# Performance work log

Measured on AMD Instinct MI355X. Metric: run time of the kernel, lower is better.

The kernel has to match this reference:

```python
import jax, jax.numpy as jnp
import numpy as np

FEATURE_COUNT = 40960
HIDDEN = 256
BATCH = 131072
BAG = 32  # active features per perspective (fixed-size bag)


def setup_inputs() -> dict:
    key = jax.random.key(0)
    ks = jax.random.split(key, 9)
    inp = {
        "indices_us": jax.random.randint(ks[0], (BATCH, BAG), 0, FEATURE_COUNT, dtype=jnp.int32),
        "indices_them": jax.random.randint(ks[1], (BATCH, BAG), 0, FEATURE_COUNT, dtype=jnp.int32),
        "emb_weight": jax.random.normal(ks[2], (FEATURE_COUNT, HIDDEN), dtype=jnp.float32) * 0.05,
        "l1_w": jax.random.normal(ks[3], (32, 2 * HIDDEN), dtype=jnp.float32) * 0.05,
        "l1_b": jax.random.normal(ks[4], (32,), dtype=jnp.float32) * 0.05,
        "l2_w": jax.random.normal(ks[5], (32, 32), dtype=jnp.float32) * 0.05,
        "l2_b": jax.random.normal(ks[6], (32,), dtype=jnp.float32) * 0.05,
        "out_w": jax.random.normal(ks[7], (1, 32), dtype=jnp.float32) * 0.05,
        "out_b": jax.random.normal(ks[8], (1,), dtype=jnp.float32) * 0.05,
    }
    return inp


def _clipped_relu(x):
    return jnp.clip(x, 0.0, 1.0)


def reference(indices_us, indices_them, emb_weight, l1_w, l1_b, l2_w, l2_b, out_w, out_b):
    # EmbeddingBag(mode='sum') with uniform bags of size BAG:
    # gather [B, BAG, H] then sum over bag dim -> [B, H]
    acc_us = emb_weight[indices_us].sum(axis=1)
    acc_them = emb_weight[indices_them].sum(axis=1)
    x = jnp.concatenate([acc_us, acc_them], axis=1)  # [B, 2H]
    x = _clipped_relu(x)
    x = _clipped_relu(x @ l1_w.T + l1_b)
    x = _clipped_relu(x @ l2_w.T + l2_b)
    return x @ out_w.T + out_b  # [B, 1]
```

## Files before the change

### kernel.cpp

```cpp
#include <hip/hip_runtime.h>
#include <hip/hip_fp16.h>


constexpr int kBatch  = 131072;
constexpr int kHidden = 256;
constexpr int kBag    = 32;
constexpr int kFeat   = 40960;

constexpr int    kSlices     = 8;
constexpr int    kSliceDims  = 32;
constexpr size_t kSliceBytes = (size_t)kFeat * kSliceDims * 2;
constexpr size_t kEmbsBytes  = kSliceBytes * kSlices;
constexpr size_t kXBytes     = (size_t)kBatch * 2 * kHidden * 2;

typedef unsigned u32x4 __attribute__((ext_vector_type(4)));

__device__ __forceinline__ float clip1(float x) {
  return fminf(fmaxf(x, 0.0f), 1.0f);
}

typedef _Float16 h2_t __attribute__((ext_vector_type(2)));

__device__ __forceinline__ unsigned pkadd(unsigned a, unsigned b) {
  const h2_t r = __builtin_bit_cast(h2_t, a) + __builtin_bit_cast(h2_t, b);
  return __builtin_bit_cast(unsigned, r);
}

__device__ __forceinline__ unsigned pkclip(unsigned a) {
  unsigned r;
  const unsigned zero = 0u;
  const unsigned one  = 0x3C003C00u;
  asm("v_pk_max_f16 %0, %1, %2\n\t"
      "v_pk_min_f16 %0, %0, %3"
      : "=&v"(r)
      : "v"(a), "v"(zero), "v"(one));
  return r;
}

__device__ __forceinline__ float fdot2w(unsigned a, unsigned b, float c) {
  return __builtin_amdgcn_fdot2(__builtin_bit_cast(h2_t, a),
                                __builtin_bit_cast(h2_t, b), c, false);
}

template <int D, int HALF>
__device__ __forceinline__ void rs_stage(float (&p)[32], int lane) {
  const bool up = (lane & D) != 0;
#pragma unroll
  for (int i = 0; i < HALF; ++i) {
    const float send = up ? p[i] : p[i + HALF];
    const float recv = __shfl_xor(send, D, 64);
    p[i] = (up ? p[i + HALF] : p[i]) + recv;
  }
}

__device__ __forceinline__ float reduce32(float (&p)[32], int lane) {
  rs_stage<32, 16>(p, lane);
  rs_stage<16, 8>(p, lane);
  rs_stage<8, 4>(p, lane);
  rs_stage<4, 2>(p, lane);
  rs_stage<2, 1>(p, lane);
  return p[0] + __shfl_xor(p[0], 1, 64);
}

__global__ void cvt_sliced(const float* __restrict__ src,
                           uint4* __restrict__ dst) {
  const int total  = kFeat * 32;
  const int stride = gridDim.x * blockDim.x;
  for (int T = blockIdx.x * blockDim.x + threadIdx.x; T < total; T += stride) {
    const int r = T >> 5, s = (T >> 2) & 7, q = T & 3;
    const float4* p = (const float4*)(src + (size_t)r * 256 + s * 32 + q * 8);
    const float4 fa = p[0], fb = p[1];
    uint4 o;
    o.x = __builtin_bit_cast(unsigned, __floats2half2_rn(fa.x, fa.y));
    o.y = __builtin_bit_cast(unsigned, __floats2half2_rn(fa.z, fa.w));
    o.z = __builtin_bit_cast(unsigned, __floats2half2_rn(fb.x, fb.y));
    o.w = __builtin_bit_cast(unsigned, __floats2half2_rn(fb.z, fb.w));
    dst[(size_t)(s * kFeat + r) * 4 + q] = o;
  }
}

__global__ void cvt_emb(const float4* __restrict__ src, uint2* __restrict__ dst) {
  const int n4 = kFeat * kHidden / 4;
  const int stride = gridDim.x * blockDim.x;
  for (int i = blockIdx.x * blockDim.x + threadIdx.x; i < n4; i += stride) {
    const float4 v = src[i];
    union { __half2 h[2]; uint2 u; } P;
    P.h[0] = __floats2half2_rn(v.x, v.y);
    P.h[1] = __floats2half2_rn(v.z, v.w);
    dst[i] = P.u;
  }
}

constexpr int kGBlocks  = 2048;
constexpr int kGTpb     = 256;
constexpr int kGChunk   = kBatch / (kGBlocks / kSlices);
constexpr int kGPerWave = kGChunk / 4;
static_assert(kGChunk * (kGBlocks / kSlices) == kBatch);
static_assert(kGPerWave % 4 == 0);

__device__ __forceinline__ void bag_reduce(const u32x4 v0, const u32x4 v1,
                                           const u32x4 v2, const u32x4 v3,
                                           int lane, unsigned& U, unsigned& T) {
  unsigned aU[4] = {pkadd(v0.x, v1.x), pkadd(v0.y, v1.y),
                    pkadd(v0.z, v1.z), pkadd(v0.w, v1.w)};
  unsigned aT[4] = {pkadd(v2.x, v3.x), pkadd(v2.y, v3.y),
                    pkadd(v2.z, v3.z), pkadd(v2.w, v3.w)};
  {
    const bool up = (lane & 4) != 0;
#pragma unroll
    for (int i = 0; i < 2; ++i) {
      unsigned sU = up ? aU[i] : aU[i + 2];
      unsigned sT = up ? aT[i] : aT[i + 2];
      sU = (unsigned)__shfl_xor((int)sU, 4, 64);
      sT = (unsigned)__shfl_xor((int)sT, 4, 64);
      aU[i] = pkadd(up ? aU[i + 2] : aU[i], sU);
      aT[i] = pkadd(up ? aT[i + 2] : aT[i], sT);
    }
  }
  {
    const bool up = (lane & 8) != 0;
    unsigned sU = up ? aU[0] : aU[1];
    unsigned sT = up ? aT[0] : aT[1];
    sU = (unsigned)__shfl_xor((int)sU, 8, 64);
    sT = (unsigned)__shfl_xor((int)sT, 8, 64);
    aU[0] = pkadd(up ? aU[1] : aU[0], sU);
    aT[0] = pkadd(up ? aT[1] : aT[0], sT);
  }
  aU[0] = pkadd(aU[0], (unsigned)__shfl_xor((int)aU[0], 16, 64));
  aT[0] = pkadd(aT[0], (unsigned)__shfl_xor((int)aT[0], 16, 64));
  aU[0] = pkadd(aU[0], (unsigned)__shfl_xor((int)aU[0], 32, 64));
  aT[0] = pkadd(aT[0], (unsigned)__shfl_xor((int)aT[0], 32, 64));
  U = aU[0];
  T = aT[0];
}

__global__ __launch_bounds__(kGTpb, 4) void nnue_gather(
    const int* __restrict__ idx_us, const int* __restrict__ idx_th,
    const __half* __restrict__ embs, __half* __restrict__ x) {
  const int s     = blockIdx.x & 7;
  const int chunk = blockIdx.x >> 3;
  const int t    = threadIdx.x;
  const int lane = t & 63;
  const int g = lane >> 2, q = lane & 3;
  const u32x4* sbase =
      (const u32x4*)((const char*)embs + (size_t)s * kSliceBytes);
  unsigned* xw = (unsigned*)x;

  const int d = q * 8 + ((lane >> 2) & 1) * 4 + ((lane >> 3) & 1) * 2;
  const int wordoff = (lane < 16 ? 0 : 128) + s * 16 + (d >> 1);

  const int b0w = chunk * kGChunk + (t >> 6) * kGPerWave;
  for (int e = 0; e < kGPerWave; e += 4) {
    const int bA = b0w + e, bB = bA + 1, bC = bA + 2, bD = bA + 3;
    const size_t oA = (size_t)bA * kBag, oB = (size_t)bB * kBag;
    const size_t oC = (size_t)bC * kBag, oD = (size_t)bD * kBag;

    const int uA0 = idx_us[oA + g], uA1 = idx_us[oA + 16 + g];
    const int tA0 = idx_th[oA + g], tA1 = idx_th[oA + 16 + g];
    const int uB0 = idx_us[oB + g], uB1 = idx_us[oB + 16 + g];
    const int tB0 = idx_th[oB + g], tB1 = idx_th[oB + 16 + g];
    const int uC0 = idx_us[oC + g], uC1 = idx_us[oC + 16 + g];
    const int tC0 = idx_th[oC + g], tC1 = idx_th[oC + 16 + g];
    const int uD0 = idx_us[oD + g], uD1 = idx_us[oD + 16 + g];
    const int tD0 = idx_th[oD + g], tD1 = idx_th[oD + 16 + g];

    const u32x4 vA0 = sbase[uA0 * 4 + q], vA1 = sbase[uA1 * 4 + q];
    const u32x4 vA2 = sbase[tA0 * 4 + q], vA3 = sbase[tA1 * 4 + q];
    const u32x4 vB0 = sbase[uB0 * 4 + q], vB1 = sbase[uB1 * 4 + q];
    const u32x4 vB2 = sbase[tB0 * 4 + q], vB3 = sbase[tB1 * 4 + q];
    const u32x4 vC0 = sbase[uC0 * 4 + q], vC1 = sbase[uC1 * 4 + q];
    const u32x4 vC2 = sbase[tC0 * 4 + q], vC3 = sbase[tC1 * 4 + q];
    const u32x4 vD0 = sbase[uD0 * 4 + q], vD1 = sbase[uD1 * 4 + q];
    const u32x4 vD2 = sbase[tD0 * 4 + q], vD3 = sbase[tD1 * 4 + q];

    unsigned UA, TA, UB, TB, UC, TC, UD, TD;
    bag_reduce(vA0, vA1, vA2, vA3, lane, UA, TA);
    bag_reduce(vB0, vB1, vB2, vB3, lane, UB, TB);
    bag_reduce(vC0, vC1, vC2, vC3, lane, UC, TC);
    bag_reduce(vD0, vD1, vD2, vD3, lane, UD, TD);

    if (lane < 32) {
      __builtin_nontemporal_store(pkclip(lane < 16 ? UA : TA),
                                  xw + (size_t)bA * 256 + wordoff);
      __builtin_nontemporal_store(pkclip(lane < 16 ? UB : TB),
                                  xw + (size_t)bB * 256 + wordoff);
      __builtin_nontemporal_store(pkclip(lane < 16 ? UC : TC),
                                  xw + (size_t)bC * 256 + wordoff);
      __builtin_nontemporal_store(pkclip(lane < 16 ? UD : TD),
                                  xw + (size_t)bD * 256 + wordoff);
    }
  }
}

constexpr int kMBlocks = 1024;
constexpr int kMTpb    = 256;
constexpr int kMWpb    = kMTpb / 64;
constexpr int kMElems  = kBatch / (kMBlocks * kMWpb);
static_assert(kBatch % (kMBlocks * kMWpb) == 0);

__global__ __launch_bounds__(kMTpb, 4) void nnue_mlp(
    const __half* __restrict__ x, const float* __restrict__ w1,
    const float* __restrict__ b1, const float* __restrict__ w2,
    const float* __restrict__ b2, const float* __restrict__ wo,
    const float* __restrict__ bo, float* __restrict__ out) {
  __shared__ __align__(16) __half sW1h[32 * 512];
  __shared__ __align__(16) __half sY1h[kMWpb][2][32];

  const int t = threadIdx.x;
  {
    const float4* src = (const float4*)w1;
#pragma unroll
    for (int c = 0; c < 16; ++c) {
      const float4 v = src[t * 16 + c];
      __half2* d = (__half2*)&sW1h[t * 64 + 4 * c];
      d[0] = __floats2half2_rn(v.x, v.y);
      d[1] = __floats2half2_rn(v.z, v.w);
    }
  }
  __syncthreads();

  const int lane   = t & 63;
  const int wlocal = t >> 6;
  const int wid    = blockIdx.x * kMWpb + wlocal;
  const int myj    = lane >> 1;
  const int j2     = lane & 31;

  const float b1r  = b1[myj];
  const float b2r  = b2[j2];
  const float wor  = wo[j2];
  const float outb = bo[0];
  unsigned w2h[16];
#pragma unroll
  for (int k = 0; k < 16; ++k) {
    w2h[k] = __builtin_bit_cast(
        unsigned, __floats2half2_rn(w2[j2 * 32 + 2 * k], w2[j2 * 32 + 2 * k + 1]));
  }

  const u32x4* xq = (const u32x4*)x;
  for (int e = 0; e < kMElems; e += 2) {
    const int b0 = wid * kMElems + e;
    const int b1i = b0 + 1;
    const u32x4 xv0 = __builtin_nontemporal_load(xq + (size_t)b0 * 64 + lane);
    const u32x4 xv1 = __builtin_nontemporal_load(xq + (size_t)b1i * 64 + lane);

    float p0[32], p1[32];
#pragma unroll
    for (int j = 0; j < 32; ++j) {
      const uint4 wv = *(const uint4*)&sW1h[(j * 64 + lane) * 8];
      float s0 = fdot2w(wv.x, xv0.x, 0.0f);
      float s1 = fdot2w(wv.x, xv1.x, 0.0f);
      s0 = fdot2w(wv.y, xv0.y, s0);
      s1 = fdot2w(wv.y, xv1.y, s1);
      s0 = fdot2w(wv.z, xv0.z, s0);
      s1 = fdot2w(wv.z, xv1.z, s1);
      s0 = fdot2w(wv.w, xv0.w, s0);
      s1 = fdot2w(wv.w, xv1.w, s1);
      p0[j] = s0;
      p1[j] = s1;
    }
    const float y10 = clip1(reduce32(p0, lane) + b1r);
    const float y11 = clip1(reduce32(p1, lane) + b1r);

    if ((lane & 1) == 0) {
      sY1h[wlocal][0][myj] = __float2half(y10);
      sY1h[wlocal][1][myj] = __float2half(y11);
    }
    asm volatile("s_waitcnt lgkmcnt(0)" ::: "memory");

    const uint4* yv0 = (const uint4*)&sY1h[wlocal][0][0];
    const uint4* yv1 = (const uint4*)&sY1h[wlocal][1][0];
    float y20 = b2r, y21 = b2r;
#pragma unroll
    for (int k4 = 0; k4 < 4; ++k4) {
      const uint4 ya = yv0[k4];
      const uint4 yb = yv1[k4];
      y20 = fdot2w(w2h[4 * k4 + 0], ya.x, y20);
      y21 = fdot2w(w2h[4 * k4 + 0], yb.x, y21);
      y20 = fdot2w(w2h[4 * k4 + 1], ya.y, y20);
      y21 = fdot2w(w2h[4 * k4 + 1], yb.y, y21);
      y20 = fdot2w(w2h[4 * k4 + 2], ya.z, y20);
      y21 = fdot2w(w2h[4 * k4 + 2], yb.z, y21);
      y20 = fdot2w(w2h[4 * k4 + 3], ya.w, y20);
      y21 = fdot2w(w2h[4 * k4 + 3], yb.w, y21);
    }
    y20 = clip1(y20);
    y21 = clip1(y21);

    float a0 = y20 * wor;
    float a1 = y21 * wor;
#pragma unroll
    for (int d = 1; d < 32; d <<= 1) {
      a0 += __shfl_xor(a0, d, 64);
      a1 += __shfl_xor(a1, d, 64);
    }
    if (lane == 0) {
      out[b0]  = a0 + outb;
      out[b1i] = a1 + outb;
    }
  }
}

constexpr int kBlocksH = 1024;
constexpr int kTpb     = 256;
constexpr int kWpb     = kTpb / 64;
constexpr int kElemsH  = kBatch / (kBlocksH * kWpb);
constexpr int kPairs   = kElemsH / 2;

__device__ __forceinline__ void mlp_tail(
    const __half* __restrict__ sW1h, __half* __restrict__ sy1row,
    const unsigned (&x2)[4], const unsigned (&w2h)[16],
    float b1r, float b2r, float wor, float outb,
    int lane, int myj, float* __restrict__ out, int b) {
  float p[32];
#pragma unroll
  for (int j = 0; j < 32; ++j) {
    const uint4 wv = *(const uint4*)&sW1h[(j * 64 + lane) * 8];
    float s = fdot2w(wv.x, x2[0], 0.0f);
    s = fdot2w(wv.y, x2[1], s);
    s = fdot2w(wv.z, x2[2], s);
    s = fdot2w(wv.w, x2[3], s);
    p[j] = s;
  }
  const float y1 = clip1(reduce32(p, lane) + b1r);

  if ((lane & 1) == 0) sy1row[myj] = __float2half(y1);
  asm volatile("s_waitcnt lgkmcnt(0)" ::: "memory");

  const uint4* yv = (const uint4*)sy1row;
  float y2 = b2r;
#pragma unroll
  for (int k4 = 0; k4 < 4; ++k4) {
    const uint4 y = yv[k4];
    y2 = fdot2w(w2h[4 * k4 + 0], y.x, y2);
    y2 = fdot2w(w2h[4 * k4 + 1], y.y, y2);
    y2 = fdot2w(w2h[4 * k4 + 2], y.z, y2);
    y2 = fdot2w(w2h[4 * k4 + 3], y.w, y2);
  }
  y2 = clip1(y2);

  float acc = y2 * wor;
#pragma unroll
  for (int d = 1; d < 32; d <<= 1) acc += __shfl_xor(acc, d, 64);
  if (lane == 0) out[b] = acc + outb;
}

__global__ __launch_bounds__(kTpb, 4) void nnue_fwd_h(
    const int* __restrict__ idx_us, const int* __restrict__ idx_th,
    const __half* __restrict__ embh, const float* __restrict__ w1,
    const float* __restrict__ b1, const float* __restrict__ w2,
    const float* __restrict__ b2, const float* __restrict__ wo,
    const float* __restrict__ bo, float* __restrict__ out) {
  __shared__ __align__(16) __half sW1h[32 * 512];
  __shared__ __align__(16) __half sY1h[kWpb][32];

  const int t = threadIdx.x;
  {
    const float4* src = (const float4*)w1;
#pragma unroll
    for (int c = 0; c < 16; ++c) {
      const float4 v = src[t * 16 + c];
      __half2* d = (__half2*)&sW1h[t * 64 + 4 * c];
      d[0] = __floats2half2_rn(v.x, v.y);
      d[1] = __floats2half2_rn(v.z, v.w);
    }
  }
  __syncthreads();

  const int lane    = t & 63;
  const int wlocal  = t >> 6;
  const int wid     = blockIdx.x * kWpb + wlocal;
  const int myj     = lane >> 1;
  const int j2      = lane & 31;
  const int half31  = lane & 31;
  const bool hiHalf = lane >= 32;
  const uint4* embq = (const uint4*)embh;

  const float b1r  = b1[myj];
  const float b2r  = b2[j2];
  const float wor  = wo[j2];
  const float outb = bo[0];
  unsigned w2h[16];
#pragma unroll
  for (int k = 0; k < 16; ++k) {
    w2h[k] = __builtin_bit_cast(
        unsigned, __floats2half2_rn(w2[j2 * 32 + 2 * k], w2[j2 * 32 + 2 * k + 1]));
  }

  for (int e = 0; e < kPairs; ++e) {
    const int b0 = wid * kElemsH + 2 * e;
    const int b1i = b0 + 1;
    const int* ip0 = (lane < kBag) ? (idx_us + (size_t)b0 * kBag + lane)
                                   : (idx_th + (size_t)b0 * kBag + (lane - kBag));
    const int* ip1 = (lane < kBag) ? (idx_us + (size_t)b1i * kBag + lane)
                                    : (idx_th + (size_t)b1i * kBag + (lane - kBag));
    const int vidx0 = *ip0;
    const int vidx1 = *ip1;

    unsigned A0[8] = {0, 0, 0, 0, 0, 0, 0, 0};
    unsigned T0[8] = {0, 0, 0, 0, 0, 0, 0, 0};
    unsigned A1[8] = {0, 0, 0, 0, 0, 0, 0, 0};
    unsigned T1[8] = {0, 0, 0, 0, 0, 0, 0, 0};
#pragma unroll
    for (int s = 0; s < 16; ++s) {
      const int r0A = __builtin_amdgcn_readlane(vidx0, 2 * s);
      const int r0B = __builtin_amdgcn_readlane(vidx0, 2 * s + 1);
      const int r1A = __builtin_amdgcn_readlane(vidx1, 2 * s);
      const int r1B = __builtin_amdgcn_readlane(vidx1, 2 * s + 1);
      const uint4 v0 = embq[(size_t)(hiHalf ? r0B : r0A) * 32 + half31];
      const uint4 v1 = embq[(size_t)(hiHalf ? r1B : r1A) * 32 + half31];
      const int o = (s & 1) * 4;
      A0[o + 0] = pkadd(A0[o + 0], v0.x);
      A0[o + 1] = pkadd(A0[o + 1], v0.y);
      A0[o + 2] = pkadd(A0[o + 2], v0.z);
      A0[o + 3] = pkadd(A0[o + 3], v0.w);
      A1[o + 0] = pkadd(A1[o + 0], v1.x);
      A1[o + 1] = pkadd(A1[o + 1], v1.y);
      A1[o + 2] = pkadd(A1[o + 2], v1.z);
      A1[o + 3] = pkadd(A1[o + 3], v1.w);
    }
#pragma unroll
    for (int s = 0; s < 16; ++s) {
      const int r0A = __builtin_amdgcn_readlane(vidx0, 32 + 2 * s);
      const int r0B = __builtin_amdgcn_readlane(vidx0, 33 + 2 * s);
      const int r1A = __builtin_amdgcn_readlane(vidx1, 32 + 2 * s);
      const int r1B = __builtin_amdgcn_readlane(vidx1, 33 + 2 * s);
      const uint4 v0 = embq[(size_t)(hiHalf ? r0B : r0A) * 32 + half31];
      const uint4 v1 = embq[(size_t)(hiHalf ? r1B : r1A) * 32 + half31];
      const int o = (s & 1) * 4;
      T0[o + 0] = pkadd(T0[o + 0], v0.x);
      T0[o + 1] = pkadd(T0[o + 1], v0.y);
      T0[o + 2] = pkadd(T0[o + 2], v0.z);
      T0[o + 3] = pkadd(T0[o + 3], v0.w);
      T1[o + 0] = pkadd(T1[o + 0], v1.x);
      T1[o + 1] = pkadd(T1[o + 1], v1.y);
      T1[o + 2] = pkadd(T1[o + 2], v1.z);
      T1[o + 3] = pkadd(T1[o + 3], v1.w);
    }

    unsigned x20[4], x21[4];
#pragma unroll
    for (int q = 0; q < 4; ++q) {
      unsigned u0 = pkadd(A0[q], A0[q + 4]);
      unsigned t0 = pkadd(T0[q], T0[q + 4]);
      unsigned u1 = pkadd(A1[q], A1[q + 4]);
      unsigned t1 = pkadd(T1[q], T1[q + 4]);
      u0 = pkadd(u0, (unsigned)__shfl_xor((int)u0, 32, 64));
      t0 = pkadd(t0, (unsigned)__shfl_xor((int)t0, 32, 64));
      u1 = pkadd(u1, (unsigned)__shfl_xor((int)u1, 32, 64));
      t1 = pkadd(t1, (unsigned)__shfl_xor((int)t1, 32, 64));
      x20[q] = pkclip(hiHalf ? t0 : u0);
      x21[q] = pkclip(hiHalf ? t1 : u1);
    }

    mlp_tail(sW1h, &sY1h[wlocal][0], x20, w2h, b1r, b2r, wor, outb, lane, myj,
             out, b0);
    mlp_tail(sW1h, &sY1h[wlocal][0], x21, w2h, b1r, b2r, wor, outb, lane, myj,
             out, b1i);
  }
}

constexpr int kTpbF    = 256;
constexpr int kWpbF    = kTpbF / 64;
constexpr int kBlocksF = 512;
constexpr int kElemsF  = kBatch / (kBlocksF * kWpbF);

__global__ __launch_bounds__(kTpbF, 2) void nnue_fwd_f32(
    const int* __restrict__ idx_us, const int* __restrict__ idx_th,
    const float* __restrict__ emb, const float* __restrict__ w1,
    const float* __restrict__ b1, const float* __restrict__ w2,
    const float* __restrict__ b2, const float* __restrict__ wo,
    const float* __restrict__ bo, float* __restrict__ out) {
  __shared__ float sW1[32][512];
  __shared__ __align__(16) float sY1[kWpbF][32];

  const int t = threadIdx.x;
  {
    const float4* src = (const float4*)w1;
    float4* dst = (float4*)&sW1[0][0];
#pragma unroll
    for (int i = 0; i < 16; ++i) dst[i * kTpbF + t] = src[i * kTpbF + t];
  }
  __syncthreads();

  const int lane   = t & 63;
  const int wlocal = t >> 6;
  const int wid    = blockIdx.x * kWpbF + wlocal;
  const int myj    = lane >> 1;
  const int j2     = lane & 31;

  const float b1r  = b1[myj];
  const float b2r  = b2[j2];
  const float wor  = wo[j2];
  const float outb = bo[0];
  float w2r[32];
#pragma unroll
  for (int k = 0; k < 32; ++k) w2r[k] = w2[j2 * 32 + k];

  for (int e = 0; e < kElemsF; ++e) {
    const int b = wid * kElemsF + e;
    const int* ip = (lane < kBag) ? (idx_us + (size_t)b * kBag + lane)
                                  : (idx_th + (size_t)b * kBag + (lane - kBag));
    const int vidx = *ip;

    float4 au = make_float4(0.f, 0.f, 0.f, 0.f);
    float4 at = make_float4(0.f, 0.f, 0.f, 0.f);
#pragma unroll
    for (int i = 0; i < kBag; ++i) {
      const int iu = __builtin_amdgcn_readlane(vidx, i);
      const float4 v = ((const float4*)(emb + (size_t)iu * kHidden))[lane];
      au.x += v.x; au.y += v.y; au.z += v.z; au.w += v.w;
    }
#pragma unroll
    for (int i = 0; i < kBag; ++i) {
      const int it2 = __builtin_amdgcn_readlane(vidx, i + kBag);
      const float4 v = ((const float4*)(emb + (size_t)it2 * kHidden))[lane];
      at.x += v.x; at.y += v.y; at.z += v.z; at.w += v.w;
    }

    au.x = clip1(au.x); au.y = clip1(au.y); au.z = clip1(au.z); au.w = clip1(au.w);
    at.x = clip1(at.x); at.y = clip1(at.y); at.z = clip1(at.z); at.w = clip1(at.w);

    float p[32];
#pragma unroll
    for (int j = 0; j < 32; ++j) {
      const float4 a = *(const float4*)&sW1[j][4 * lane];
      const float4 c = *(const float4*)&sW1[j][kHidden + 4 * lane];
      p[j] = au.x * a.x + au.y * a.y + au.z * a.z + au.w * a.w +
             at.x * c.x + at.y * c.y + at.z * c.z + at.w * c.w;
    }
    const float y1 = clip1(reduce32(p, lane) + b1r);

    if ((lane & 1) == 0) sY1[wlocal][myj] = y1;
    asm volatile("s_waitcnt lgkmcnt(0)" ::: "memory");

    const float4* y4 = (const float4*)&sY1[wlocal][0];
    float y2 = b2r;
#pragma unroll
    for (int k4 = 0; k4 < 8; ++k4) {
      const float4 y = y4[k4];
      y2 += w2r[4 * k4 + 0] * y.x + w2r[4 * k4 + 1] * y.y +
            w2r[4 * k4 + 2] * y.z + w2r[4 * k4 + 3] * y.w;
    }
    y2 = clip1(y2);

    float acc = y2 * wor;
#pragma unroll
    for (int d = 1; d < 32; d <<= 1) acc += __shfl_xor(acc, d, 64);
    if (lane == 0) out[b] = acc + outb;
  }
}

extern "C" void kernel_launch(void* const* d_in, const int* in_sizes, int n_in,
                              void* d_out, int out_size, void* d_ws, size_t ws_size,
                              hipStream_t stream) {
  const int* idx_us  = (const int*)d_in[0];
  const int* idx_th  = (const int*)d_in[1];
  const float* emb   = (const float*)d_in[2];
  const float* w1    = (const float*)d_in[3];
  const float* b1    = (const float*)d_in[4];
  const float* w2    = (const float*)d_in[5];
  const float* b2    = (const float*)d_in[6];
  const float* wo    = (const float*)d_in[7];
  const float* bo    = (const float*)d_in[8];
  float* out         = (float*)d_out;

  if (ws_size >= kEmbsBytes + kXBytes) {
    __half* embs = (__half*)d_ws;
    __half* x    = (__half*)((char*)d_ws + kEmbsBytes);
    cvt_sliced<<<2560, 256, 0, stream>>>(emb, (uint4*)embs);
    nnue_gather<<<kGBlocks, kGTpb, 0, stream>>>(idx_us, idx_th, embs, x);
    nnue_mlp<<<kMBlocks, kMTpb, 0, stream>>>(x, w1, b1, w2, b2, wo, bo, out);
  } else if (ws_size >= kEmbsBytes) {
    __half* embh = (__half*)d_ws;
    cvt_emb<<<2048, 256, 0, stream>>>((const float4*)emb, (uint2*)embh);
    nnue_fwd_h<<<kBlocksH, kTpb, 0, stream>>>(idx_us, idx_th, embh, w1, b1, w2,
                                              b2, wo, bo, out);
  } else {
    nnue_fwd_f32<<<kBlocksF, kTpbF, 0, stream>>>(idx_us, idx_th, emb, w1, b1,
                                                 w2, b2, wo, bo, out);
  }
}
```

Baseline: 404.2 us.

## Software-pipeline gather loads across element pairs and double MLP grid blocks

Restructures the gather loop into a two-stage software pipeline: the loads for the next pair of batch elements are issued before the current pair is reduced and stored, so memory latency overlaps with the shuffle reductions. On the last iteration it prefetches element 0 again, a wasted load. It also doubles the MLP kernel's block count, halving the elements per wave and meaning the W1 staging into shared memory is repeated by twice as many blocks. Register pressure rises from holding two pairs of loaded vectors at once.

```diff
diff --git a/kernel.cpp b/kernel.cpp
--- a/kernel.cpp
+++ b/kernel.cpp
@@ -134,6 +134,41 @@
   T = aT[0];
 }
 
+__device__ __forceinline__ void g_load2(const int* __restrict__ idx_us,
+                                        const int* __restrict__ idx_th,
+                                        const u32x4* __restrict__ sbase,
+                                        int g, int q, int bA, u32x4 (&V)[8]) {
+  const int bB = bA + 1;
+  const size_t oA = (size_t)bA * kBag, oB = (size_t)bB * kBag;
+  const int uA0 = idx_us[oA + g], uA1 = idx_us[oA + 16 + g];
+  const int tA0 = idx_th[oA + g], tA1 = idx_th[oA + 16 + g];
+  const int uB0 = idx_us[oB + g], uB1 = idx_us[oB + 16 + g];
+  const int tB0 = idx_th[oB + g], tB1 = idx_th[oB + 16 + g];
+  V[0] = sbase[uA0 * 4 + q];
+  V[1] = sbase[uA1 * 4 + q];
+  V[2] = sbase[tA0 * 4 + q];
+  V[3] = sbase[tA1 * 4 + q];
+  V[4] = sbase[uB0 * 4 + q];
+  V[5] = sbase[uB1 * 4 + q];
+  V[6] = sbase[tB0 * 4 + q];
+  V[7] = sbase[tB1 * 4 + q];
+}
+
+__device__ __forceinline__ void g_finish2(const u32x4 (&V)[8], int lane,
+                                          int bA, unsigned* __restrict__ xw,
+                                          int wordoff) {
+  const int bB = bA + 1;
+  unsigned UA, TA, UB, TB;
+  bag_reduce(V[0], V[1], V[2], V[3], lane, UA, TA);
+  bag_reduce(V[4], V[5], V[6], V[7], lane, UB, TB);
+  if (lane < 32) {
+    __builtin_nontemporal_store(pkclip(lane < 16 ? UA : TA),
+                                xw + (size_t)bA * 256 + wordoff);
+    __builtin_nontemporal_store(pkclip(lane < 16 ? UB : TB),
+                                xw + (size_t)bB * 256 + wordoff);
+  }
+}
+
 __global__ __launch_bounds__(kGTpb, 4) void nnue_gather(
     const int* __restrict__ idx_us, const int* __restrict__ idx_th,
     const __half* __restrict__ embs, __half* __restrict__ x) {
@@ -150,49 +185,20 @@
   const int wordoff = (lane < 16 ? 0 : 128) + s * 16 + (d >> 1);
 
   const int b0w = chunk * kGChunk + (t >> 6) * kGPerWave;
+
+  u32x4 P[8], Q[8];
+  g_load2(idx_us, idx_th, sbase, g, q, b0w, P);
   for (int e = 0; e < kGPerWave; e += 4) {
-    const int bA = b0w + e, bB = bA + 1, bC = bA + 2, bD = bA + 3;
-    const size_t oA = (size_t)bA * kBag, oB = (size_t)bB * kBag;
-    const size_t oC = (size_t)bC * kBag, oD = (size_t)bD * kBag;
-
-    const int uA0 = idx_us[oA + g], uA1 = idx_us[oA + 16 + g];
-    const int tA0 = idx_th[oA + g], tA1 = idx_th[oA + 16 + g];
-    const int uB0 = idx_us[oB + g], uB1 = idx_us[oB + 16 + g];
-    const int tB0 = idx_th[oB + g], tB1 = idx_th[oB + 16 + g];
-    const int uC0 = idx_us[oC + g], uC1 = idx_us[oC + 16 + g];
-    const int tC0 = idx_th[oC + g], tC1 = idx_th[oC + 16 + g];
-    const int uD0 = idx_us[oD + g], uD1 = idx_us[oD + 16 + g];
-    const int tD0 = idx_th[oD + g], tD1 = idx_th[oD + 16 + g];
-
-    const u32x4 vA0 = sbase[uA0 * 4 + q], vA1 = sbase[uA1 * 4 + q];
-    const u32x4 vA2 = sbase[tA0 * 4 + q], vA3 = sbase[tA1 * 4 + q];
-    const u32x4 vB0 = sbase[uB0 * 4 + q], vB1 = sbase[uB1 * 4 + q];
-    const u32x4 vB2 = sbase[tB0 * 4 + q], vB3 = sbase[tB1 * 4 + q];
-    const u32x4 vC0 = sbase[uC0 * 4 + q], vC1 = sbase[uC1 * 4 + q];
-    const u32x4 vC2 = sbase[tC0 * 4 + q], vC3 = sbase[tC1 * 4 + q];
-    const u32x4 vD0 = sbase[uD0 * 4 + q], vD1 = sbase[uD1 * 4 + q];
-    const u32x4 vD2 = sbase[tD0 * 4 + q], vD3 = sbase[tD1 * 4 + q];
-
-    unsigned UA, TA, UB, TB, UC, TC, UD, TD;
-    bag_reduce(vA0, vA1, vA2, vA3, lane, UA, TA);
-    bag_reduce(vB0, vB1, vB2, vB3, lane, UB, TB);
-    bag_reduce(vC0, vC1, vC2, vC3, lane, UC, TC);
-    bag_reduce(vD0, vD1, vD2, vD3, lane, UD, TD);
-
-    if (lane < 32) {
-      __builtin_nontemporal_store(pkclip(lane < 16 ? UA : TA),
-                                  xw + (size_t)bA * 256 + wordoff);
-      __builtin_nontemporal_store(pkclip(lane < 16 ? UB : TB),
-                                  xw + (size_t)bB * 256 + wordoff);
-      __builtin_nontemporal_store(pkclip(lane < 16 ? UC : TC),
-                                  xw + (size_t)bC * 256 + wordoff);
-      __builtin_nontemporal_store(pkclip(lane < 16 ? UD : TD),
-                                  xw + (size_t)bD * 256 + wordoff);
-    }
-  }
-}
-
-constexpr int kMBlocks = 1024;
+    const int bA = b0w + e;
+    g_load2(idx_us, idx_th, sbase, g, q, bA + 2, Q);
+    g_finish2(P, lane, bA, xw, wordoff);
+    const int eN = (e + 4 < kGPerWave) ? (e + 4) : 0;
+    g_load2(idx_us, idx_th, sbase, g, q, b0w + eN, P);
+    g_finish2(Q, lane, bA + 2, xw, wordoff);
+  }
+}
+
+constexpr int kMBlocks = 2048;
 constexpr int kMTpb    = 256;
 constexpr int kMWpb    = kMTpb / 64;
 constexpr int kMElems  = kBatch / (kMBlocks * kMWpb);
```

New measurement: 405.1 us. About the same (+0.2%).
